# Kernel tuning notes

Hardware: AMD Instinct MI355X
Metric: run time of the kernel (lower is better)

Reference implementation:

```python
import jax, jax.numpy as jnp
import numpy as np

B, N, NFEAT, NHID, NOUT = 16, 2048, 128, 128, 64
BN_EPS = 1e-5
LRELU_ALPHA = 0.2


def setup_inputs() -> dict:
    key = jax.random.key(0)
    ks = jax.random.split(key, 6)
    stdv = 1.0 / np.sqrt(NHID)
    return {
        "x": jax.random.normal(ks[0], (B, N, NFEAT), dtype=jnp.float32),
        "adj": jnp.zeros((N, N), dtype=jnp.float32),  # passed to GAT but unused
        "adj_gcn": jax.random.uniform(ks[1], (N, N), dtype=jnp.float32),
        "gcn_weight": jax.random.uniform(ks[2], (NFEAT, NHID), minval=-stdv, maxval=stdv, dtype=jnp.float32),
        "gcn_bias": jax.random.uniform(ks[3], (NHID,), minval=-stdv, maxval=stdv, dtype=jnp.float32),
        "bn_gamma": jnp.ones((NHID,), dtype=jnp.float32),
        "bn_beta": jnp.zeros((NHID,), dtype=jnp.float32),
        "gat_W": jax.random.normal(ks[4], (NFEAT, NOUT), dtype=jnp.float32) * 0.05,
    }


def reference(x, adj, adj_gcn, gcn_weight, gcn_bias, bn_gamma, bn_beta, gat_W):
    # --- GCN layer: adj @ (x @ W) + b ---
    support = jnp.einsum("bnc,cd->bnd", x, gcn_weight)
    h = jnp.einsum("nm,bmd->bnd", adj_gcn, support) + gcn_bias  # [B,N,nhid]
    # --- BatchNorm1d (training mode: batch stats over B,N per channel) ---
    mean = h.mean(axis=(0, 1))
    var = h.var(axis=(0, 1))
    h = (h - mean) * jax.lax.rsqrt(var + BN_EPS) * bn_gamma + bn_beta
    # --- ReLU ---
    h = jax.nn.relu(h)
    # --- GAT layer (adj arg unused, as in original) ---
    h_prime = jnp.einsum("bnd,de->bne", h, gat_W)  # [B,N,nout]
    e = jnp.einsum("bne,bme->bnm", h_prime, h_prime)  # [B,N,N]
    e = jnp.where(e > 0, e, LRELU_ALPHA * e)  # LeakyReLU(0.2)
    attention = jax.nn.softmax(e, axis=1)  # softmax over dim=1 (as in source)
    # repeat-mul-sum over dim=2 reduces exactly to row-sum scaling of h_prime
    out = h_prime * attention.sum(axis=2, keepdims=True)  # [B,N,nout]
    return out
```

## Files before the change

### kernel.cpp

```cpp
#include <hip/hip_runtime.h>
#include <math.h>

#define NB 16
#define NN 2048
#define NF 128
#define NH 128
#define NO 64

typedef short bf16x8 __attribute__((ext_vector_type(8)));
typedef float f32x4 __attribute__((ext_vector_type(4)));
typedef unsigned short u16;
typedef unsigned int u32;

#define LOG2E 1.4426950408889634f
#define EXPSHIFT 43.28085122666891f

__device__ __forceinline__ u16 f2bf(float f) {
  u32 u = __builtin_bit_cast(u32, f);
  return (u16)((u + 0x7fffu + ((u >> 16) & 1u)) >> 16);
}
__device__ __forceinline__ float bf2f(u16 h) {
  u32 u = ((u32)h) << 16;
  return __builtin_bit_cast(float, u);
}

__device__ __forceinline__ void gload16(const void* g, void* l) {
  __builtin_amdgcn_global_load_lds((const __attribute__((address_space(1))) void*)g,
                                   (__attribute__((address_space(3))) void*)l, 16, 0, 0);
}
__device__ __forceinline__ f32x4 mfma16(bf16x8 a, bf16x8 b, f32x4 c) {
  return __builtin_amdgcn_mfma_f32_16x16x32_bf16(a, b, c, 0, 0, 0);
}
__device__ __forceinline__ float explr(float z) {
  return __builtin_amdgcn_exp2f(fmaf(fmaxf(z, 0.2f * z), LOG2E, -EXPSHIFT));
}

__global__ __launch_bounds__(256) void k_prep(const float* __restrict__ x,
                                              const float* __restrict__ adj,
                                              const float* __restrict__ gcn_w,
                                              const float* __restrict__ gat_w,
                                              u16* __restrict__ suppT_sw,
                                              u16* __restrict__ adj_sw,
                                              u16* __restrict__ Wg_sw) {
  __shared__ __align__(16) u16 ts[64 * 136];
  __shared__ __align__(16) u16 Bs[16384];
  const int t = threadIdx.x;
  const int bid = blockIdx.x;
  if (bid == 0) {
#pragma unroll
    for (int it = 0; it < 4; ++it) {
      const int s = t + it * 256;
      const int kb = s >> 6, col = s & 63;
      u16 tmp[8];
#pragma unroll
      for (int j = 0; j < 8; ++j) tmp[j] = f2bf(gat_w[(kb * 8 + j) * 64 + col]);
      uint4 o;
      o.x = (u32)tmp[0] | ((u32)tmp[1] << 16);
      o.y = (u32)tmp[2] | ((u32)tmp[3] << 16);
      o.z = (u32)tmp[4] | ((u32)tmp[5] << 16);
      o.w = (u32)tmp[6] | ((u32)tmp[7] << 16);
      *(uint4*)&Wg_sw[(size_t)s * 8] = o;
    }
  } else if (bid < 1025) {
    const int tile = bid - 1;
    const int n0 = (tile >> 5) * 64, m0 = (tile & 31) * 64;
#pragma unroll
    for (int k = 0; k < 4; ++k) {
      const int s = t + k * 256;
      const int row = s >> 4, c4 = (s & 15) * 4;
      const float4 f = *(const float4*)&adj[(size_t)(n0 + row) * 2048 + m0 + c4];
      uint2 pk;
      pk.x = (u32)f2bf(f.x) | ((u32)f2bf(f.y) << 16);
      pk.y = (u32)f2bf(f.z) | ((u32)f2bf(f.w) << 16);
      *(uint2*)&ts[row * 136 + c4] = pk;
    }
    __syncthreads();
#pragma unroll
    for (int k = 0; k < 2; ++k) {
      const int s = t + k * 256;
      const int kb = s >> 6, row = s & 63;
      const uint4 v = *(const uint4*)&ts[row * 136 + kb * 8];
      *(uint4*)&adj_sw[(size_t)tile * 4096 + (size_t)s * 8] = v;
    }
  } else {
    const int sb = bid - 1025;
    const int m0g = sb * 64;
    const int w = t >> 6, l = t & 63;
    const int lg = l >> 4, lr = l & 15;
#pragma unroll
    for (int i = 0; i < 8; ++i) {
      const int s = t + i * 256;
      const int kb = s >> 7, d = s & 127;
      u16 tmp[8];
#pragma unroll
      for (int j = 0; j < 8; ++j) tmp[j] = f2bf(gcn_w[(kb * 8 + j) * 128 + d]);
      uint4 o;
      o.x = (u32)tmp[0] | ((u32)tmp[1] << 16);
      o.y = (u32)tmp[2] | ((u32)tmp[3] << 16);
      o.z = (u32)tmp[4] | ((u32)tmp[5] << 16);
      o.w = (u32)tmp[6] | ((u32)tmp[7] << 16);
      *(uint4*)&Bs[(size_t)s * 8] = o;
    }
#pragma unroll
    for (int k = 0; k < 8; ++k) {
      const int s = t + k * 256;
      const int row = s >> 5, c4 = (s & 31) * 4;
      const float4 f = *(const float4*)&x[(size_t)(m0g + row) * 128 + c4];
      uint2 pk;
      pk.x = (u32)f2bf(f.x) | ((u32)f2bf(f.y) << 16);
      pk.y = (u32)f2bf(f.z) | ((u32)f2bf(f.w) << 16);
      *(uint2*)&ts[row * 136 + c4] = pk;
    }
    __syncthreads();
    f32x4 acc[8];
#pragma unroll
    for (int nf = 0; nf < 8; ++nf) {
      acc[nf][0] = 0.f; acc[nf][1] = 0.f;
      acc[nf][2] = 0.f; acc[nf][3] = 0.f;
    }
#pragma unroll
    for (int ks = 0; ks < 4; ++ks) {
      const int kb = ks * 4 + lg;
      const bf16x8 a = *(const bf16x8*)&ts[(w * 16 + lr) * 136 + kb * 8];
#pragma unroll
      for (int nf = 0; nf < 8; ++nf) {
        const bf16x8 bb = *(const bf16x8*)&Bs[((size_t)kb * 128 + nf * 16 + lr) * 8];
        acc[nf] = mfma16(a, bb, acc[nf]);
      }
    }
    __syncthreads();
    u16* os = Bs;
#pragma unroll
    for (int nf = 0; nf < 8; ++nf) {
      const int d = nf * 16 + lr;
      const int mb = w * 16 + lg * 4;
      const u32 p0 = (u32)f2bf(acc[nf][0]) | ((u32)f2bf(acc[nf][1]) << 16);
      const u32 p1 = (u32)f2bf(acc[nf][2]) | ((u32)f2bf(acc[nf][3]) << 16);
      *(u32*)&os[d * 72 + mb] = p0;
      *(u32*)&os[d * 72 + mb + 2] = p1;
    }
    __syncthreads();
    const int b = m0g >> 11, mt = (m0g & 2047) >> 6;
#pragma unroll
    for (int i = 0; i < 4; ++i) {
      const int s = i * 256 + t;
      const int kb = s >> 7, d = s & 127;
      const uint4 v = *(const uint4*)&os[d * 72 + kb * 8];
      *(uint4*)&suppT_sw[((size_t)((b * 32 + mt) * 8 + kb)) * 1024 + (size_t)d * 8] = v;
    }
  }
}

__global__ __launch_bounds__(512) void k_gcn(const u16* __restrict__ adj_sw,
                                             const u16* __restrict__ suppT_sw,
                                             const float* __restrict__ bias,
                                             float* __restrict__ h,
                                             float* __restrict__ psum,
                                             float* __restrict__ psq) {
  const int flat = blockIdx.y * 32 + blockIdx.x;
  const int nf2 = (flat & 7) * 64 + (flat >> 3);
  const int b = nf2 >> 5, nt = nf2 & 31;
  const int n0 = nt * 64;
  const int t = threadIdx.x;
  const int w = t >> 6, l = t & 63;
  const int wm = w >> 1, wn = w & 1;
  const int lg = l >> 4, lr = l & 15;
  __shared__ __align__(16) u16 As[2][4096];
  __shared__ __align__(16) u16 Bs[2][8192];
  __shared__ float redS[4][128], redQ[4][128];

  f32x4 acc[4];
#pragma unroll
  for (int nf = 0; nf < 4; ++nf) {
    acc[nf][0] = 0.f; acc[nf][1] = 0.f;
    acc[nf][2] = 0.f; acc[nf][3] = 0.f;
  }

#define GCN_STAGE(buf, kt)                                                        \
  {                                                                               \
    gload16(adj_sw + ((size_t)(nt * 32 + (kt))) * 4096 + (size_t)t * 8,           \
            &As[buf][t * 8]);                                                     \
    _Pragma("unroll") for (int i = 0; i < 2; ++i) {                               \
      const int s = i * 512 + t;                                                  \
      gload16(suppT_sw + ((size_t)(b * 32 + (kt))) * 8192 + (size_t)s * 8,        \
              &Bs[buf][s * 8]);                                                   \
    }                                                                             \
  }

  GCN_STAGE(0, 0);
  __syncthreads();
  for (int kt = 0; kt < 32; ++kt) {
    const int cur = kt & 1;
    if (kt + 1 < 32) GCN_STAGE(cur ^ 1, kt + 1);
#pragma unroll
    for (int kb = 0; kb < 2; ++kb) {
      const int ko = kb * 4 + lg;
      const bf16x8 a0 = *(const bf16x8*)&As[cur][(ko * 64 + wm * 16 + lr) * 8];
      const bf16x8 b0 = *(const bf16x8*)&Bs[cur][(ko * 128 + wn * 64 + lr) * 8];
      const bf16x8 b1 = *(const bf16x8*)&Bs[cur][(ko * 128 + wn * 64 + 16 + lr) * 8];
      const bf16x8 b2 = *(const bf16x8*)&Bs[cur][(ko * 128 + wn * 64 + 32 + lr) * 8];
      const bf16x8 b3 = *(const bf16x8*)&Bs[cur][(ko * 128 + wn * 64 + 48 + lr) * 8];
      acc[0] = mfma16(a0, b0, acc[0]);
      acc[1] = mfma16(a0, b1, acc[1]);
      acc[2] = mfma16(a0, b2, acc[2]);
      acc[3] = mfma16(a0, b3, acc[3]);
    }
    __syncthreads();
  }
#undef GCN_STAGE
#pragma unroll
  for (int nf = 0; nf < 4; ++nf) {
    const int d = wn * 64 + nf * 16 + lr;
    const float bv = bias[d];
    float s = 0.f, q = 0.f;
#pragma unroll
    for (int r = 0; r < 4; ++r) {
      const float v = acc[nf][r] + bv;
      const int row = n0 + wm * 16 + lg * 4 + r;
      h[((size_t)(b * NN + row)) * NH + d] = v;
      s += v;
      q = fmaf(v, v, q);
    }
    s += __shfl_xor(s, 16);
    s += __shfl_xor(s, 32);
    q += __shfl_xor(q, 16);
    q += __shfl_xor(q, 32);
    if (lg == 0) {
      redS[wm][d] = s;
      redQ[wm][d] = q;
    }
  }
  __syncthreads();
  if (t < 128) {
    const int blk = b * 32 + nt;
    psum[blk * 128 + t] = redS[0][t] + redS[1][t] + redS[2][t] + redS[3][t];
    psq[blk * 128 + t] = redQ[0][t] + redQ[1][t] + redQ[2][t] + redQ[3][t];
  }
}

__global__ __launch_bounds__(1024) void k_bnstat2(const float* __restrict__ psum,
                                                  const float* __restrict__ psq,
                                                  const float* __restrict__ gamma,
                                                  const float* __restrict__ beta,
                                                  float* __restrict__ scale,
                                                  float* __restrict__ shift) {
  const int t = threadIdx.x;
  const int d = t & 127;
  const int g = t >> 7;
  float s = 0.f, q = 0.f;
  for (int i = g; i < 512; i += 8) {
    s += psum[i * 128 + d];
    q += psq[i * 128 + d];
  }
  __shared__ float ls[8][128], lq[8][128];
  ls[g][d] = s;
  lq[g][d] = q;
  __syncthreads();
  if (t < 128) {
    s = 0.f;
    q = 0.f;
#pragma unroll
    for (int i = 0; i < 8; ++i) {
      s += ls[i][t];
      q += lq[i][t];
    }
    const float inv = 1.f / (float)(NB * NN);
    const float mean = s * inv;
    const float var = q * inv - mean * mean;
    const float sc = gamma[t] * rsqrtf(var + 1e-5f);
    scale[t] = sc;
    shift[t] = beta[t] - mean * sc;
  }
}

__global__ __launch_bounds__(256) void k_hp(const float* __restrict__ h,
                                            const float* __restrict__ scale,
                                            const float* __restrict__ shift,
                                            const u16* __restrict__ Wg_sw,
                                            u16* __restrict__ hp_sw) {
  const int row0 = blockIdx.x * 64;
  const int t = threadIdx.x, w = t >> 6, l = t & 63;
  const int lg = l >> 4, lr = l & 15;
  __shared__ __align__(16) u16 him[8192];
  __shared__ __align__(16) u16 Wg[8192];
  __shared__ __align__(16) u16 hos[64][72];
  __shared__ float scs[128], shs[128];
#pragma unroll
  for (int i = 0; i < 4; ++i) {
    const int s0 = i * 256 + w * 64;
    gload16(Wg_sw + (size_t)(s0 + l) * 8, &Wg[(size_t)s0 * 8]);
  }
  if (t < 128) {
    scs[t] = scale[t];
    shs[t] = shift[t];
  }
  __syncthreads();
#pragma unroll
  for (int k = 0; k < 4; ++k) {
    const int s = t + k * 256;
    const int row = s >> 4, kb = s & 15;
    const float4 v0 = *(const float4*)&h[(size_t)(row0 + row) * NH + kb * 8];
    const float4 v1 = *(const float4*)&h[(size_t)(row0 + row) * NH + kb * 8 + 4];
    u16 p[8];
    p[0] = f2bf(fmaxf(fmaf(v0.x, scs[kb * 8 + 0], shs[kb * 8 + 0]), 0.f));
    p[1] = f2bf(fmaxf(fmaf(v0.y, scs[kb * 8 + 1], shs[kb * 8 + 1]), 0.f));
    p[2] = f2bf(fmaxf(fmaf(v0.z, scs[kb * 8 + 2], shs[kb * 8 + 2]), 0.f));
    p[3] = f2bf(fmaxf(fmaf(v0.w, scs[kb * 8 + 3], shs[kb * 8 + 3]), 0.f));
    p[4] = f2bf(fmaxf(fmaf(v1.x, scs[kb * 8 + 4], shs[kb * 8 + 4]), 0.f));
    p[5] = f2bf(fmaxf(fmaf(v1.y, scs[kb * 8 + 5], shs[kb * 8 + 5]), 0.f));
    p[6] = f2bf(fmaxf(fmaf(v1.z, scs[kb * 8 + 6], shs[kb * 8 + 6]), 0.f));
    p[7] = f2bf(fmaxf(fmaf(v1.w, scs[kb * 8 + 7], shs[kb * 8 + 7]), 0.f));
    uint4 o;
    o.x = (u32)p[0] | ((u32)p[1] << 16);
    o.y = (u32)p[2] | ((u32)p[3] << 16);
    o.z = (u32)p[4] | ((u32)p[5] << 16);
    o.w = (u32)p[6] | ((u32)p[7] << 16);
    const int boff = (row * 256 + kb * 16) ^ ((row & 7) << 4);
    *(uint4*)&him[boff >> 1] = o;
  }
  __syncthreads();
  f32x4 acc[4];
#pragma unroll
  for (int nf = 0; nf < 4; ++nf) {
    acc[nf][0] = 0.f; acc[nf][1] = 0.f;
    acc[nf][2] = 0.f; acc[nf][3] = 0.f;
  }
#pragma unroll
  for (int kks = 0; kks < 4; ++kks) {
    const int ko = kks * 4 + lg;
    const int arow = w * 16 + lr;
    const int aoff = (arow * 256 + ko * 16) ^ ((arow & 7) << 4);
    const bf16x8 a = *(const bf16x8*)&him[aoff >> 1];
#pragma unroll
    for (int nf = 0; nf < 4; ++nf) {
      const bf16x8 bfr = *(const bf16x8*)&Wg[(ko * 64 + nf * 16 + lr) * 8];
      acc[nf] = mfma16(a, bfr, acc[nf]);
    }
  }
#pragma unroll
  for (int nf = 0; nf < 4; ++nf) {
    const int col = nf * 16 + lr;
#pragma unroll
    for (int r = 0; r < 4; ++r) {
      hos[w * 16 + lg * 4 + r][col] = f2bf(acc[nf][r]);
    }
  }
  __syncthreads();
  const size_t tbase = (size_t)blockIdx.x * 4096;
#pragma unroll
  for (int k = 0; k < 2; ++k) {
    const int s = t + k * 256;
    const int kb = s >> 6, r6 = s & 63;
    const uint2 lo = *(const uint2*)&hos[r6][kb * 8];
    const uint2 hi = *(const uint2*)&hos[r6][kb * 8 + 4];
    uint4 o;
    o.x = lo.x; o.y = lo.y; o.z = hi.x; o.w = hi.y;
    *(uint4*)&hp_sw[tbase + kb * 512 + r6 * 8] = o;
  }
}

__device__ __forceinline__ void attn_swz(int& b, int& nt, int& qtr) {
  const int flat = blockIdx.y * 512 + blockIdx.x;
  const int lf = (flat & 7) * 256 + (flat >> 3);
  b = lf >> 7;
  const int rem = lf & 127;
  qtr = rem >> 5;
  nt = rem & 31;
}

__global__ __launch_bounds__(256) void k_attnA(const u16* __restrict__ hp_sw,
                                               float* __restrict__ Dpart) {
  int b, nt, qtr;
  attn_swz(b, nt, qtr);
  const int t = threadIdx.x, w = t >> 6, l = t & 63;
  const int lg = l >> 4, lr = l & 15;
  const u16* rbase = hp_sw + (size_t)(b * 32 + nt) * 4096;
  const int qrow = (w << 4) + lr;
  const bf16x8 bq0 = *(const bf16x8*)&rbase[(lg * 64 + qrow) * 8];
  const bf16x8 bq1 = *(const bf16x8*)&rbase[((lg + 4) * 64 + qrow) * 8];
  const u16* cb = hp_sw + (size_t)(b * 32 + qtr * 8) * 4096;
  float S = 0.f;
#pragma unroll 2
  for (int mt = 0; mt < 8; ++mt) {
    const u16* base = cb + (size_t)mt * 4096;
#pragma unroll
    for (int mf = 0; mf < 4; ++mf) {
      const bf16x8 a0 = *(const bf16x8*)&base[(lg * 64 + mf * 16 + lr) * 8];
      const bf16x8 a1 = *(const bf16x8*)&base[((lg + 4) * 64 + mf * 16 + lr) * 8];
      f32x4 z;
      z[0] = 0.f; z[1] = 0.f; z[2] = 0.f; z[3] = 0.f;
      __builtin_amdgcn_s_setprio(1);
      z = mfma16(a0, bq0, z);
      z = mfma16(a1, bq1, z);
      __builtin_amdgcn_s_setprio(0);
      S += explr(z[0]) + explr(z[1]) + explr(z[2]) + explr(z[3]);
    }
  }
  S += __shfl_xor(S, 16);
  S += __shfl_xor(S, 32);
  if (l < 16) Dpart[qtr * 32768 + b * NN + nt * 64 + qrow] = S;
}

__global__ __launch_bounds__(256) void k_attnB(const u16* __restrict__ hp_sw,
                                               const float* __restrict__ Dpart,
                                               float* __restrict__ Spart) {
  int b, nt, qtr;
  attn_swz(b, nt, qtr);
  const int t = threadIdx.x, w = t >> 6, l = t & 63;
  const int lg = l >> 4, lr = l & 15;
  __shared__ float iDs[512];
  const u16* rbase = hp_sw + (size_t)(b * 32 + nt) * 4096;
  const int qrow = (w << 4) + lr;
  const bf16x8 bq0 = *(const bf16x8*)&rbase[(lg * 64 + qrow) * 8];
  const bf16x8 bq1 = *(const bf16x8*)&rbase[((lg + 4) * 64 + qrow) * 8];
  const u16* cb = hp_sw + (size_t)(b * 32 + qtr * 8) * 4096;
#pragma unroll
  for (int i = 0; i < 2; ++i) {
    const int idx = t + i * 256;
    const int n = b * NN + qtr * 512 + idx;
    iDs[idx] = 1.f / (Dpart[n] + Dpart[32768 + n] + Dpart[65536 + n] + Dpart[98304 + n]);
  }
  __syncthreads();
  float S = 0.f;
#pragma unroll 2
  for (int mt = 0; mt < 8; ++mt) {
    const u16* base = cb + (size_t)mt * 4096;
#pragma unroll
    for (int mf = 0; mf < 4; ++mf) {
      const bf16x8 a0 = *(const bf16x8*)&base[(lg * 64 + mf * 16 + lr) * 8];
      const bf16x8 a1 = *(const bf16x8*)&base[((lg + 4) * 64 + mf * 16 + lr) * 8];
      f32x4 z;
      z[0] = 0.f; z[1] = 0.f; z[2] = 0.f; z[3] = 0.f;
      __builtin_amdgcn_s_setprio(1);
      z = mfma16(a0, bq0, z);
      z = mfma16(a1, bq1, z);
      __builtin_amdgcn_s_setprio(0);
      const float4 dv = *(const float4*)&iDs[mt * 64 + mf * 16 + lg * 4];
      S = fmaf(explr(z[0]), dv.x, S);
      S = fmaf(explr(z[1]), dv.y, S);
      S = fmaf(explr(z[2]), dv.z, S);
      S = fmaf(explr(z[3]), dv.w, S);
    }
  }
  S += __shfl_xor(S, 16);
  S += __shfl_xor(S, 32);
  if (l < 16) Spart[qtr * 32768 + b * NN + nt * 64 + qrow] = S;
}

__global__ __launch_bounds__(256) void k_scale(const u16* __restrict__ hp_sw,
                                               const float* __restrict__ Spart,
                                               float* __restrict__ out) {
  const int bx = blockIdx.x;
  const int b = bx >> 5, nt = bx & 31;
  const int t = threadIdx.x;
  __shared__ float Sv[64];
  if (t < 64) {
    const int n = b * NN + nt * 64 + t;
    Sv[t] = Spart[n] + Spart[32768 + n] + Spart[65536 + n] + Spart[98304 + n];
  }
  __syncthreads();
  const u16* rbase = hp_sw + (size_t)(b * 32 + nt) * 4096;
  const int row = t >> 2;
  const float sc = Sv[row];
  const size_t R = (size_t)b * NN + nt * 64 + row;
#pragma unroll
  for (int hh = 0; hh < 2; ++hh) {
    const int kb = (t & 3) * 2 + hh;
    const uint4 v = *(const uint4*)&rbase[(kb * 64 + row) * 8];
    float4 o0, o1;
    o0.x = bf2f((u16)(v.x & 0xffff)) * sc;
    o0.y = bf2f((u16)(v.x >> 16)) * sc;
    o0.z = bf2f((u16)(v.y & 0xffff)) * sc;
    o0.w = bf2f((u16)(v.y >> 16)) * sc;
    o1.x = bf2f((u16)(v.z & 0xffff)) * sc;
    o1.y = bf2f((u16)(v.z >> 16)) * sc;
    o1.z = bf2f((u16)(v.w & 0xffff)) * sc;
    o1.w = bf2f((u16)(v.w >> 16)) * sc;
    *(float4*)&out[R * NO + kb * 8] = o0;
    *(float4*)&out[R * NO + kb * 8 + 4] = o1;
  }
}

extern "C" void kernel_launch(void* const* d_in, const int* in_sizes, int n_in,
                              void* d_out, int out_size, void* d_ws, size_t ws_size,
                              hipStream_t stream) {
  const float* x = (const float*)d_in[0];
  const float* adj_gcn = (const float*)d_in[2];
  const float* gcn_w = (const float*)d_in[3];
  const float* gcn_b = (const float*)d_in[4];
  const float* gamma = (const float*)d_in[5];
  const float* beta = (const float*)d_in[6];
  const float* gat_w = (const float*)d_in[7];
  float* out = (float*)d_out;
  float* ws = (float*)d_ws;

  u16* adj_sw = (u16*)ws;
  u16* suppT_sw = (u16*)(ws + 2097152);
  float* hbuf = ws + 4194304;
  u16* hp_sw = (u16*)(ws + 8388608);
  float* psum = ws + 9437184;
  float* psq = psum + 65536;
  float* scale = psq + 65536;
  float* shift = scale + 128;
  u16* Wg_sw = (u16*)(shift + 128);
  float* Dpart = ws + 9617664;
  float* Spart = Dpart + 131072;

  k_prep<<<dim3(1537), dim3(256), 0, stream>>>(x, adj_gcn, gcn_w, gat_w, suppT_sw, adj_sw, Wg_sw);
  k_gcn<<<dim3(32, 16), dim3(512), 0, stream>>>(adj_sw, suppT_sw, gcn_b, hbuf, psum, psq);
  k_bnstat2<<<dim3(1), dim3(1024), 0, stream>>>(psum, psq, gamma, beta, scale, shift);
  k_hp<<<dim3(512), dim3(256), 0, stream>>>(hbuf, scale, shift, Wg_sw, hp_sw);
  k_attnA<<<dim3(512, 4), dim3(256), 0, stream>>>(hp_sw, Dpart);
  k_attnB<<<dim3(512, 4), dim3(256), 0, stream>>>(hp_sw, Dpart, Spart);
  k_scale<<<dim3(512), dim3(256), 0, stream>>>(hp_sw, Spart, out);
}
```

Before: 110.3 us.

## Fuse output scaling into attention pass B with 512-thread blocks over full columns

The second attention pass now runs one 512-thread block per 64-row tile. Each half of the block covers half of the 2048 columns instead of splitting columns across four blocks. The two halves combine their row sums in shared memory and the block writes the scaled output directly, which removes the Spart buffer and the separate k_scale launch. The trade-off is 512 blocks instead of 2048 (less parallelism and coarser tail), and each block loads 2048 inverse denominators into shared memory.

```diff
diff --git a/kernel.cpp b/kernel.cpp
--- a/kernel.cpp
+++ b/kernel.cpp
@@ -359,19 +359,13 @@
   }
 }
 
-__device__ __forceinline__ void attn_swz(int& b, int& nt, int& qtr) {
+__global__ __launch_bounds__(256) void k_attnA(const u16* __restrict__ hp_sw,
+                                               float* __restrict__ Dpart) {
   const int flat = blockIdx.y * 512 + blockIdx.x;
   const int lf = (flat & 7) * 256 + (flat >> 3);
-  b = lf >> 7;
-  const int rem = lf & 127;
-  qtr = rem >> 5;
-  nt = rem & 31;
-}
-
-__global__ __launch_bounds__(256) void k_attnA(const u16* __restrict__ hp_sw,
-                                               float* __restrict__ Dpart) {
-  int b, nt, qtr;
-  attn_swz(b, nt, qtr);
+  const int b = lf >> 7;
+  const int qtr = (lf & 127) >> 5;
+  const int nt = lf & 31;
   const int t = threadIdx.x, w = t >> 6, l = t & 63;
   const int lg = l >> 4, lr = l & 15;
   const u16* rbase = hp_sw + (size_t)(b * 32 + nt) * 4096;
@@ -401,29 +395,33 @@
   if (l < 16) Dpart[qtr * 32768 + b * NN + nt * 64 + qrow] = S;
 }
 
-__global__ __launch_bounds__(256) void k_attnB(const u16* __restrict__ hp_sw,
+__global__ __launch_bounds__(512) void k_attnB(const u16* __restrict__ hp_sw,
                                                const float* __restrict__ Dpart,
-                                               float* __restrict__ Spart) {
-  int b, nt, qtr;
-  attn_swz(b, nt, qtr);
+                                               float* __restrict__ out) {
+  const int flat = blockIdx.x;
+  const int lf = (flat & 7) * 64 + (flat >> 3);
+  const int b = lf >> 5, nt = lf & 31;
   const int t = threadIdx.x, w = t >> 6, l = t & 63;
   const int lg = l >> 4, lr = l & 15;
-  __shared__ float iDs[512];
+  const int wr = w & 3;
+  const int wh = w >> 2;
+  __shared__ float iDs[2048];
+  __shared__ float Sv[2][64];
   const u16* rbase = hp_sw + (size_t)(b * 32 + nt) * 4096;
-  const int qrow = (w << 4) + lr;
+  const int qrow = (wr << 4) + lr;
   const bf16x8 bq0 = *(const bf16x8*)&rbase[(lg * 64 + qrow) * 8];
   const bf16x8 bq1 = *(const bf16x8*)&rbase[((lg + 4) * 64 + qrow) * 8];
-  const u16* cb = hp_sw + (size_t)(b * 32 + qtr * 8) * 4096;
-#pragma unroll
-  for (int i = 0; i < 2; ++i) {
-    const int idx = t + i * 256;
-    const int n = b * NN + qtr * 512 + idx;
+#pragma unroll
+  for (int i = 0; i < 4; ++i) {
+    const int idx = t + i * 512;
+    const int n = b * NN + idx;
     iDs[idx] = 1.f / (Dpart[n] + Dpart[32768 + n] + Dpart[65536 + n] + Dpart[98304 + n]);
   }
   __syncthreads();
+  const u16* cb = hp_sw + (size_t)(b * 32 + wh * 16) * 4096;
   float S = 0.f;
 #pragma unroll 2
-  for (int mt = 0; mt < 8; ++mt) {
+  for (int mt = 0; mt < 16; ++mt) {
     const u16* base = cb + (size_t)mt * 4096;
 #pragma unroll
     for (int mf = 0; mf < 4; ++mf) {
@@ -435,7 +433,7 @@
       z = mfma16(a0, bq0, z);
       z = mfma16(a1, bq1, z);
       __builtin_amdgcn_s_setprio(0);
-      const float4 dv = *(const float4*)&iDs[mt * 64 + mf * 16 + lg * 4];
+      const float4 dv = *(const float4*)&iDs[wh * 1024 + mt * 64 + mf * 16 + lg * 4];
       S = fmaf(explr(z[0]), dv.x, S);
       S = fmaf(explr(z[1]), dv.y, S);
       S = fmaf(explr(z[2]), dv.z, S);
@@ -444,41 +442,24 @@
   }
   S += __shfl_xor(S, 16);
   S += __shfl_xor(S, 32);
-  if (l < 16) Spart[qtr * 32768 + b * NN + nt * 64 + qrow] = S;
-}
-
-__global__ __launch_bounds__(256) void k_scale(const u16* __restrict__ hp_sw,
-                                               const float* __restrict__ Spart,
-                                               float* __restrict__ out) {
-  const int bx = blockIdx.x;
-  const int b = bx >> 5, nt = bx & 31;
-  const int t = threadIdx.x;
-  __shared__ float Sv[64];
-  if (t < 64) {
-    const int n = b * NN + nt * 64 + t;
-    Sv[t] = Spart[n] + Spart[32768 + n] + Spart[65536 + n] + Spart[98304 + n];
-  }
-  __syncthreads();
-  const u16* rbase = hp_sw + (size_t)(b * 32 + nt) * 4096;
-  const int row = t >> 2;
-  const float sc = Sv[row];
+  if (l < 16) Sv[wh][qrow] = S;
+  __syncthreads();
+  const int row = t >> 3;
+  const int kb = t & 7;
+  const float sc = Sv[0][row] + Sv[1][row];
   const size_t R = (size_t)b * NN + nt * 64 + row;
-#pragma unroll
-  for (int hh = 0; hh < 2; ++hh) {
-    const int kb = (t & 3) * 2 + hh;
-    const uint4 v = *(const uint4*)&rbase[(kb * 64 + row) * 8];
-    float4 o0, o1;
-    o0.x = bf2f((u16)(v.x & 0xffff)) * sc;
-    o0.y = bf2f((u16)(v.x >> 16)) * sc;
-    o0.z = bf2f((u16)(v.y & 0xffff)) * sc;
-    o0.w = bf2f((u16)(v.y >> 16)) * sc;
-    o1.x = bf2f((u16)(v.z & 0xffff)) * sc;
-    o1.y = bf2f((u16)(v.z >> 16)) * sc;
-    o1.z = bf2f((u16)(v.w & 0xffff)) * sc;
-    o1.w = bf2f((u16)(v.w >> 16)) * sc;
-    *(float4*)&out[R * NO + kb * 8] = o0;
-    *(float4*)&out[R * NO + kb * 8 + 4] = o1;
-  }
+  const uint4 v = *(const uint4*)&rbase[(kb * 64 + row) * 8];
+  float4 o0, o1;
+  o0.x = bf2f((u16)(v.x & 0xffff)) * sc;
+  o0.y = bf2f((u16)(v.x >> 16)) * sc;
+  o0.z = bf2f((u16)(v.y & 0xffff)) * sc;
+  o0.w = bf2f((u16)(v.y >> 16)) * sc;
+  o1.x = bf2f((u16)(v.z & 0xffff)) * sc;
+  o1.y = bf2f((u16)(v.z >> 16)) * sc;
+  o1.z = bf2f((u16)(v.w & 0xffff)) * sc;
+  o1.w = bf2f((u16)(v.w >> 16)) * sc;
+  *(float4*)&out[R * NO + kb * 8] = o0;
+  *(float4*)&out[R * NO + kb * 8 + 4] = o1;
 }
 
 extern "C" void kernel_launch(void* const* d_in, const int* in_sizes, int n_in,
@@ -504,13 +485,11 @@
   float* shift = scale + 128;
   u16* Wg_sw = (u16*)(shift + 128);
   float* Dpart = ws + 9617664;
-  float* Spart = Dpart + 131072;
 
   k_prep<<<dim3(1537), dim3(256), 0, stream>>>(x, adj_gcn, gcn_w, gat_w, suppT_sw, adj_sw, Wg_sw);
   k_gcn<<<dim3(32, 16), dim3(512), 0, stream>>>(adj_sw, suppT_sw, gcn_b, hbuf, psum, psq);
   k_bnstat2<<<dim3(1), dim3(1024), 0, stream>>>(psum, psq, gamma, beta, scale, shift);
   k_hp<<<dim3(512), dim3(256), 0, stream>>>(hbuf, scale, shift, Wg_sw, hp_sw);
   k_attnA<<<dim3(512, 4), dim3(256), 0, stream>>>(hp_sw, Dpart);
-  k_attnB<<<dim3(512, 4), dim3(256), 0, stream>>>(hp_sw, Dpart, Spart);
-  k_scale<<<dim3(512), dim3(256), 0, stream>>>(hp_sw, Spart, out);
-}
+  k_attnB<<<dim3(512), dim3(512), 0, stream>>>(hp_sw, Dpart, out);
+}
```

Result: faster. 107.2 us (-2.8%).
